# Optimization experiments

Measured on AMD Instinct MI355X. Metric: run time of the kernel, lower is better.

## Reference

```python
import jax, jax.numpy as jnp
import numpy as np

NB_CLASSES = 8192
SZ_EMBED = 64
SMOOTHING = 0.1


def setup_inputs() -> dict:
    key = jax.random.key(0)
    k1, k2, k3 = jax.random.split(key, 3)
    X = jax.random.normal(k1, (8192, SZ_EMBED), dtype=jnp.float32)
    T = jax.random.randint(k2, (8192,), 0, NB_CLASSES)
    proxies = jax.random.normal(k3, (NB_CLASSES, SZ_EMBED), dtype=jnp.float32) / 8.0
    return {"X": X, "T": T, "proxies": proxies}


def reference(X, T, proxies):
    # L2-normalize and scale by 3 (as in the torch module)
    Xn = 3.0 * X / jnp.linalg.norm(X, axis=-1, keepdims=True)   # [N, E]
    Pn = 3.0 * proxies / jnp.linalg.norm(proxies, axis=-1, keepdims=True)  # [C, E]

    # squared pairwise distances D[i, c] = ||Xn_i - Pn_c||^2, computed once
    x_sq = jnp.sum(Xn * Xn, axis=-1, keepdims=True)             # [N, 1]
    p_sq = jnp.sum(Pn * Pn, axis=-1)                            # [C]
    D = x_sq + p_sq[None, :] - 2.0 * jnp.einsum('ne,ce->nc', Xn, Pn)  # [N, C]

    # out[i, c] = log( exp(D[i, c]) / sum_c' exp(D[i, c']) )
    out = D - jax.nn.logsumexp(D, axis=-1, keepdims=True)       # [N, C]

    # binarize + smooth labels
    nb_classes = proxies.shape[0]
    onehot = T[:, None] == jnp.arange(nb_classes)[None, :]      # [N, C] bool
    Tm = jnp.where(onehot, 1.0 - SMOOTHING, SMOOTHING / (nb_classes - 1)).astype(X.dtype)

    loss = jnp.mean(jnp.sum(-Tm * out, axis=-1))
    return loss
```

## Files before the change

kernel.cpp:

```cpp
#include <hip/hip_runtime.h>
#include <math.h>

#define NR 8192
#define NC 8192
#define EE 64
#define LOG2E 1.4426950408889634f

typedef __attribute__((ext_vector_type(8))) short bf16x8;
typedef __attribute__((ext_vector_type(4))) float f32x4;

__device__ __forceinline__ float bf2f(unsigned short u) {
    unsigned int x = ((unsigned int)u) << 16;
    return __builtin_bit_cast(float, x);
}
__device__ __forceinline__ unsigned short f2bf(float f) {
    unsigned int u = __builtin_bit_cast(unsigned int, f);
    u += 0x7FFFu + ((u >> 16) & 1u);
    return (unsigned short)(u >> 16);
}

__global__ __launch_bounds__(256) void norm_kernel(
    const float* __restrict__ X, const float* __restrict__ P,
    unsigned short* __restrict__ Xb, unsigned short* __restrict__ Pb)
{
    int row  = blockIdx.x * 4 + (threadIdx.x >> 6);
    int lane = threadIdx.x & 63;
    bool isX = row < NR;
    int r = isX ? row : row - NR;
    const float* src = isX ? X : P;
    float v = src[(size_t)r * EE + lane];
    float s = v * v;
    #pragma unroll
    for (int off = 32; off; off >>= 1) s += __shfl_xor(s, off);
    float xn = v * (3.0f * rsqrtf(s));
    (isX ? Xb : Pb)[(size_t)r * EE + lane] = f2bf(xn);
}

__global__ __launch_bounds__(256) void colsum_kernel(
    const unsigned short* __restrict__ Pb, float* __restrict__ sumPn)
{
    int w = threadIdx.x >> 6, l = threadIdx.x & 63;
    float acc = 0.f;
    int rbase = blockIdx.x * 128 + w * 32;
    for (int i = 0; i < 32; ++i)
        acc += bf2f(Pb[(size_t)(rbase + i) * EE + l]);
    __shared__ float red[4][64];
    red[w][l] = acc;
    __syncthreads();
    if (w == 0)
        atomicAdd(&sumPn[l], red[0][l] + red[1][l] + red[2][l] + red[3][l]);
}

__global__ __launch_bounds__(256) void main_kernel(
    const unsigned short* __restrict__ Xb, const unsigned short* __restrict__ Pb,
    float* __restrict__ rowSumExp)
{
    const int tid = threadIdx.x;
    const int w  = tid >> 6, l = tid & 63;
    const int lr = l & 15, lg = l >> 4;
    const int r0 = blockIdx.x * 64;
    const int cbase = blockIdx.y * 512;

    bf16x8 a[4][2];
    #pragma unroll
    for (int rt = 0; rt < 4; ++rt)
        #pragma unroll
        for (int kk = 0; kk < 2; ++kk)
            a[rt][kk] = *reinterpret_cast<const bf16x8*>(
                Xb + (size_t)(r0 + rt * 16 + lr) * EE + kk * 32 + lg * 8);

    float accE[4][4] = {};
    const float KN  = -2.0f * LOG2E;
    const float C18 = 18.0f * LOG2E;

    #pragma unroll 2
    for (int j = 0; j < 8; ++j) {
        const int c0 = cbase + (j * 4 + w) * 16;
        const size_t bb = (size_t)(c0 + lr) * EE + lg * 8;
        bf16x8 b0 = *reinterpret_cast<const bf16x8*>(Pb + bb);
        bf16x8 b1 = *reinterpret_cast<const bf16x8*>(Pb + bb + 32);
        #pragma unroll
        for (int rt = 0; rt < 4; ++rt) {
            f32x4 d = {0.f, 0.f, 0.f, 0.f};
            d = __builtin_amdgcn_mfma_f32_16x16x32_bf16(a[rt][0], b0, d, 0, 0, 0);
            d = __builtin_amdgcn_mfma_f32_16x16x32_bf16(a[rt][1], b1, d, 0, 0, 0);
            #pragma unroll
            for (int q = 0; q < 4; ++q)
                accE[rt][q] += __builtin_exp2f(fmaf(KN, d[q], C18));
        }
    }

    #pragma unroll
    for (int rt = 0; rt < 4; ++rt)
        #pragma unroll
        for (int q = 0; q < 4; ++q) {
            float v = accE[rt][q];
            v += __shfl_xor(v, 1);
            v += __shfl_xor(v, 2);
            v += __shfl_xor(v, 4);
            v += __shfl_xor(v, 8);
            if (lr == 0)
                atomicAdd(&rowSumExp[r0 + rt * 16 + lg * 4 + q], v);
        }
}

__global__ __launch_bounds__(1024) void final_kernel(
    const unsigned short* __restrict__ Xb, const unsigned short* __restrict__ Pb,
    const int* __restrict__ T, const float* __restrict__ sumPn,
    const float* __restrict__ rowSumExp, float* __restrict__ out)
{
    __shared__ float terms[16];
    int wid = threadIdx.x >> 6, lane = threadIdx.x & 63;
    float sp = sumPn[lane];
    float wsum = 0.f;
    #pragma unroll
    for (int rr = 0; rr < 4; ++rr) {
        int row = blockIdx.x * 64 + wid * 4 + rr;
        int t = T[row];
        float x  = bf2f(Xb[(size_t)row * EE + lane]);
        float pt = bf2f(Pb[(size_t)t  * EE + lane]);
        float d1 = x * pt;
        float d2 = x * sp;
        #pragma unroll
        for (int off = 32; off; off >>= 1) {
            d1 += __shfl_xor(d1, off);
            d2 += __shfl_xor(d2, off);
        }
        if (lane == 0) {
            float Dt   = 18.0f - 2.0f * d1;
            float sumD = (float)NC * 18.0f - 2.0f * d2;
            float lse  = __logf(rowSumExp[row]);
            wsum += lse - (0.9f * Dt + (0.1f / 8191.0f) * (sumD - Dt));
        }
    }
    if (lane == 0) terms[wid] = wsum;
    __syncthreads();
    if (threadIdx.x == 0) {
        float s = 0.f;
        #pragma unroll
        for (int i = 0; i < 16; ++i) s += terms[i];
        atomicAdd(out, s * (1.0f / (float)NR));
    }
}

extern "C" void kernel_launch(void* const* d_in, const int* in_sizes, int n_in,
                              void* d_out, int out_size, void* d_ws, size_t ws_size,
                              hipStream_t stream)
{
    const float* X = (const float*)d_in[0];
    const int*   T = (const int*)d_in[1];
    const float* P = (const float*)d_in[2];

    unsigned short* Xb = (unsigned short*)d_ws;
    unsigned short* Pb = Xb + (size_t)NR * EE;
    float* rowSumExp = (float*)(Pb + (size_t)NC * EE);
    float* sumPn     = rowSumExp + NR;
    float* out       = (float*)d_out;

    hipMemsetAsync(rowSumExp, 0, (size_t)(NR + 64) * sizeof(float), stream);
    hipMemsetAsync(out, 0, sizeof(float), stream);

    norm_kernel<<<(NR + NC) / 4, 256, 0, stream>>>(X, P, Xb, Pb);
    colsum_kernel<<<64, 256, 0, stream>>>(Pb, sumPn);
    main_kernel<<<dim3(NR / 64, 16), 256, 0, stream>>>(Xb, Pb, rowSumExp);
    final_kernel<<<NR / 64, 1024, 0, stream>>>(Xb, Pb, T, sumPn, rowSumExp, out);
}
```

Measured before the change: 55.32 us.

## Prescale X into MFMA operand, drop atomics and memsets via partial buffers

Stores a second copy of normalized X prescaled by -2*log2e and seeds the MFMA accumulator with 18*log2e, so the exponent argument comes straight out of the matrix op without a per-element FMA. The main kernel's work split changes: each wave now owns 64 rows over a 256-column slice across 32 splits, and writes per-split partial sums instead of doing atomics. Column sums and the final loss also use partial buffers plus a small reduce kernel, which removes both memsets and all atomics. The cost is an extra X buffer write, one more launch, and slightly lower precision because the scale is folded into the bf16 operand.

```diff
diff --git a/kernel.cpp b/kernel.cpp
--- a/kernel.cpp
+++ b/kernel.cpp
@@ -4,7 +4,11 @@
 #define NR 8192
 #define NC 8192
 #define EE 64
-#define LOG2E 1.4426950408889634f
+#define LOG2E   1.4426950408889634f
+#define KSCALE  (-2.0f * LOG2E)
+#define C18     (18.0f * LOG2E)
+#define NSPLIT  32
+#define CPS     (NC / NSPLIT)
 
 typedef __attribute__((ext_vector_type(8))) short bf16x8;
 typedef __attribute__((ext_vector_type(4))) float f32x4;
@@ -21,7 +25,8 @@
 
 __global__ __launch_bounds__(256) void norm_kernel(
     const float* __restrict__ X, const float* __restrict__ P,
-    unsigned short* __restrict__ Xb, unsigned short* __restrict__ Pb)
+    unsigned short* __restrict__ Xb, unsigned short* __restrict__ Xs,
+    unsigned short* __restrict__ Pb)
 {
     int row  = blockIdx.x * 4 + (threadIdx.x >> 6);
     int lane = threadIdx.x & 63;
@@ -33,11 +38,16 @@
     #pragma unroll
     for (int off = 32; off; off >>= 1) s += __shfl_xor(s, off);
     float xn = v * (3.0f * rsqrtf(s));
-    (isX ? Xb : Pb)[(size_t)r * EE + lane] = f2bf(xn);
+    if (isX) {
+        Xb[(size_t)r * EE + lane] = f2bf(xn);
+        Xs[(size_t)r * EE + lane] = f2bf(xn * KSCALE);
+    } else {
+        Pb[(size_t)r * EE + lane] = f2bf(xn);
+    }
 }
 
 __global__ __launch_bounds__(256) void colsum_kernel(
-    const unsigned short* __restrict__ Pb, float* __restrict__ sumPn)
+    const unsigned short* __restrict__ Pb, float* __restrict__ sumPnPart)
 {
     int w = threadIdx.x >> 6, l = threadIdx.x & 63;
     float acc = 0.f;
@@ -48,18 +58,20 @@
     red[w][l] = acc;
     __syncthreads();
     if (w == 0)
-        atomicAdd(&sumPn[l], red[0][l] + red[1][l] + red[2][l] + red[3][l]);
+        sumPnPart[blockIdx.x * 64 + l] =
+            red[0][l] + red[1][l] + red[2][l] + red[3][l];
 }
 
 __global__ __launch_bounds__(256) void main_kernel(
-    const unsigned short* __restrict__ Xb, const unsigned short* __restrict__ Pb,
-    float* __restrict__ rowSumExp)
+    const unsigned short* __restrict__ Xs, const unsigned short* __restrict__ Pb,
+    float* __restrict__ ePart)
 {
     const int tid = threadIdx.x;
     const int w  = tid >> 6, l = tid & 63;
     const int lr = l & 15, lg = l >> 4;
-    const int r0 = blockIdx.x * 64;
-    const int cbase = blockIdx.y * 512;
+    const int r0 = blockIdx.x * 256 + w * 64;
+    const int cbase = blockIdx.y * CPS;
+    const int s = blockIdx.y;
 
     bf16x8 a[4][2];
     #pragma unroll
@@ -67,26 +79,25 @@
         #pragma unroll
         for (int kk = 0; kk < 2; ++kk)
             a[rt][kk] = *reinterpret_cast<const bf16x8*>(
-                Xb + (size_t)(r0 + rt * 16 + lr) * EE + kk * 32 + lg * 8);
+                Xs + (size_t)(r0 + rt * 16 + lr) * EE + kk * 32 + lg * 8);
 
     float accE[4][4] = {};
-    const float KN  = -2.0f * LOG2E;
-    const float C18 = 18.0f * LOG2E;
+    const f32x4 dinit = {C18, C18, C18, C18};
 
     #pragma unroll 2
-    for (int j = 0; j < 8; ++j) {
-        const int c0 = cbase + (j * 4 + w) * 16;
+    for (int j = 0; j < CPS / 16; ++j) {
+        const int c0 = cbase + j * 16;
         const size_t bb = (size_t)(c0 + lr) * EE + lg * 8;
         bf16x8 b0 = *reinterpret_cast<const bf16x8*>(Pb + bb);
         bf16x8 b1 = *reinterpret_cast<const bf16x8*>(Pb + bb + 32);
         #pragma unroll
         for (int rt = 0; rt < 4; ++rt) {
-            f32x4 d = {0.f, 0.f, 0.f, 0.f};
+            f32x4 d = dinit;
             d = __builtin_amdgcn_mfma_f32_16x16x32_bf16(a[rt][0], b0, d, 0, 0, 0);
             d = __builtin_amdgcn_mfma_f32_16x16x32_bf16(a[rt][1], b1, d, 0, 0, 0);
             #pragma unroll
             for (int q = 0; q < 4; ++q)
-                accE[rt][q] += __builtin_exp2f(fmaf(KN, d[q], C18));
+                accE[rt][q] += __builtin_exp2f(d[q]);
         }
     }
 
@@ -100,18 +111,27 @@
             v += __shfl_xor(v, 4);
             v += __shfl_xor(v, 8);
             if (lr == 0)
-                atomicAdd(&rowSumExp[r0 + rt * 16 + lg * 4 + q], v);
+                ePart[(size_t)(r0 + rt * 16 + lg * 4 + q) * NSPLIT + s] = v;
         }
 }
 
 __global__ __launch_bounds__(1024) void final_kernel(
     const unsigned short* __restrict__ Xb, const unsigned short* __restrict__ Pb,
-    const int* __restrict__ T, const float* __restrict__ sumPn,
-    const float* __restrict__ rowSumExp, float* __restrict__ out)
-{
+    const int* __restrict__ T, const float* __restrict__ sumPnPart,
+    const float* __restrict__ ePart, float* __restrict__ lossPart)
+{
+    __shared__ float spn[64];
     __shared__ float terms[16];
     int wid = threadIdx.x >> 6, lane = threadIdx.x & 63;
-    float sp = sumPn[lane];
+
+    if (threadIdx.x < 64) {
+        float s = 0.f;
+        for (int b = 0; b < 64; ++b) s += sumPnPart[b * 64 + threadIdx.x];
+        spn[threadIdx.x] = s;
+    }
+    __syncthreads();
+
+    float sp = spn[lane];
     float wsum = 0.f;
     #pragma unroll
     for (int rr = 0; rr < 4; ++rr) {
@@ -121,15 +141,17 @@
         float pt = bf2f(Pb[(size_t)t  * EE + lane]);
         float d1 = x * pt;
         float d2 = x * sp;
+        float es = (lane < NSPLIT) ? ePart[(size_t)row * NSPLIT + lane] : 0.f;
         #pragma unroll
         for (int off = 32; off; off >>= 1) {
             d1 += __shfl_xor(d1, off);
             d2 += __shfl_xor(d2, off);
+            es += __shfl_xor(es, off);
         }
         if (lane == 0) {
             float Dt   = 18.0f - 2.0f * d1;
             float sumD = (float)NC * 18.0f - 2.0f * d2;
-            float lse  = __logf(rowSumExp[row]);
+            float lse  = __logf(es);
             wsum += lse - (0.9f * Dt + (0.1f / 8191.0f) * (sumD - Dt));
         }
     }
@@ -139,8 +161,22 @@
         float s = 0.f;
         #pragma unroll
         for (int i = 0; i < 16; ++i) s += terms[i];
-        atomicAdd(out, s * (1.0f / (float)NR));
-    }
+        lossPart[blockIdx.x] = s;
+    }
+}
+
+__global__ __launch_bounds__(128) void reduce_kernel(
+    const float* __restrict__ lossPart, float* __restrict__ out)
+{
+    __shared__ float red[2];
+    int w = threadIdx.x >> 6, l = threadIdx.x & 63;
+    float v = lossPart[threadIdx.x];
+    #pragma unroll
+    for (int off = 32; off; off >>= 1) v += __shfl_xor(v, off);
+    if (l == 0) red[w] = v;
+    __syncthreads();
+    if (threadIdx.x == 0)
+        out[0] = (red[0] + red[1]) * (1.0f / (float)NR);
 }
 
 extern "C" void kernel_launch(void* const* d_in, const int* in_sizes, int n_in,
@@ -152,16 +188,16 @@
     const float* P = (const float*)d_in[2];
 
     unsigned short* Xb = (unsigned short*)d_ws;
-    unsigned short* Pb = Xb + (size_t)NR * EE;
-    float* rowSumExp = (float*)(Pb + (size_t)NC * EE);
-    float* sumPn     = rowSumExp + NR;
+    unsigned short* Xs = Xb + (size_t)NR * EE;
+    unsigned short* Pb = Xs + (size_t)NR * EE;
+    float* ePart     = (float*)(Pb + (size_t)NC * EE);
+    float* sumPnPart = ePart + (size_t)NR * NSPLIT;
+    float* lossPart  = sumPnPart + 64 * 64;
     float* out       = (float*)d_out;
 
-    hipMemsetAsync(rowSumExp, 0, (size_t)(NR + 64) * sizeof(float), stream);
-    hipMemsetAsync(out, 0, sizeof(float), stream);
-
-    norm_kernel<<<(NR + NC) / 4, 256, 0, stream>>>(X, P, Xb, Pb);
-    colsum_kernel<<<64, 256, 0, stream>>>(Pb, sumPn);
-    main_kernel<<<dim3(NR / 64, 16), 256, 0, stream>>>(Xb, Pb, rowSumExp);
-    final_kernel<<<NR / 64, 1024, 0, stream>>>(Xb, Pb, T, sumPn, rowSumExp, out);
-}
+    norm_kernel<<<(NR + NC) / 4, 256, 0, stream>>>(X, P, Xb, Xs, Pb);
+    colsum_kernel<<<64, 256, 0, stream>>>(Pb, sumPnPart);
+    main_kernel<<<dim3(NR / 256, NSPLIT), 256, 0, stream>>>(Xs, Pb, ePart);
+    final_kernel<<<NR / 64, 1024, 0, stream>>>(Xb, Pb, T, sumPnPart, ePart, lossPart);
+    reduce_kernel<<<1, 128, 0, stream>>>(lossPart, out);
+}
```

Result: faster. 47.96 us (-13.3%).
